# Optimization experiments

Measured on AMD Instinct MI355X. Metric: run time of the kernel, lower is better.

Reference implementation:

```python
import jax, jax.numpy as jnp
import numpy as np

VOXEL_SIZE = np.array([0.1, 0.1, 0.2], np.float32)
PC_RANGE = np.array([-51.2, -51.2, -5.0, 51.2, 51.2, 3.0], np.float32)
MAX_POINTS = 32
MAX_VOXELS = 60000  # training cap (max_voxels[0])
GRID = np.round((PC_RANGE[3:] - PC_RANGE[:3]) / VOXEL_SIZE).astype(np.int64)  # [1024,1024,40]
N_POINTS = 1_200_000


def setup_inputs() -> dict:
    key = jax.random.key(0)
    k1, k2 = jax.random.split(key)
    lo = jnp.asarray(PC_RANGE[:3] - 2.0)   # slight margin -> some out-of-range points get dropped
    hi = jnp.asarray(PC_RANGE[3:] + 2.0)
    xyz = jax.random.uniform(k1, (N_POINTS, 3), minval=lo, maxval=hi)
    feat = jax.random.uniform(k2, (N_POINTS, 1))  # reflectivity
    return {"points": jnp.concatenate([xyz, feat], axis=1)}


def reference(points):
    # Hard voxelization (deterministic): first-occurrence voxel ordering,
    # first max_points points kept per voxel, capped at max_voxels.
    # Outputs padded to static MAX_VOXELS; voxel_num gives the valid count.
    N, ndim = points.shape
    gx, gy, gz = int(GRID[0]), int(GRID[1]), int(GRID[2])
    sentinel = gx * gy * gz  # flat id for out-of-range points (sorts last)

    vs = jnp.asarray(VOXEL_SIZE)
    rmin = jnp.asarray(PC_RANGE[:3])
    c = jnp.floor((points[:, :3] - rmin) / vs).astype(jnp.int32)  # [N,3] (x,y,z)
    valid = jnp.all((c >= 0) & (c < jnp.asarray(GRID, jnp.int32)), axis=1)
    flat = jnp.where(valid, (c[:, 0] * gy + c[:, 1]) * gz + c[:, 2], sentinel)

    # stable sort -> within a voxel, points keep original order
    order = jnp.argsort(flat, stable=True)
    sflat = flat[order]
    svalid = valid[order]

    new_seg = jnp.concatenate([jnp.array([True]), sflat[1:] != sflat[:-1]])
    seg_id = jnp.cumsum(new_seg) - 1                      # segment index per sorted point
    pos = jnp.arange(N)
    seg_start = jax.lax.cummax(jnp.where(new_seg, pos, 0), axis=0)
    rank = pos - seg_start                                # slot of point within its voxel

    seg_rep = jax.ops.segment_min(order, seg_id, num_segments=N)          # first-occurrence point idx
    seg_count = jax.ops.segment_sum(svalid.astype(jnp.int32), seg_id, num_segments=N)
    seg_exists = seg_count > 0                            # real (in-range) voxel segments

    # order voxels by first occurrence (matches deterministic CUDA kernel)
    rep_key = jnp.where(seg_exists, seg_rep, N)
    vox_order = jnp.argsort(rep_key, stable=True)
    vid = jnp.zeros(N, jnp.int32).at[vox_order].set(jnp.arange(N, dtype=jnp.int32))

    # scatter points into [MAX_VOXELS, MAX_POINTS, ndim]
    pv = vid[seg_id]
    keep = svalid & (pv < MAX_VOXELS) & (rank < MAX_POINTS)
    pv_s = jnp.where(keep, pv, MAX_VOXELS)  # OOB -> dropped
    voxels = jnp.zeros((MAX_VOXELS, MAX_POINTS, ndim), points.dtype)
    voxels = voxels.at[pv_s, jnp.minimum(rank, MAX_POINTS - 1)].set(points[order], mode='drop')

    # per-voxel outputs
    seg_vid = jnp.where(seg_exists, vid, MAX_VOXELS)
    npv = jnp.zeros(MAX_VOXELS, jnp.int32).at[seg_vid].set(
        jnp.minimum(seg_count, MAX_POINTS), mode='drop')
    seg_flat = jax.ops.segment_min(sflat, seg_id, num_segments=N)
    zc = seg_flat % gz
    yc = (seg_flat // gz) % gy
    xc = seg_flat // (gy * gz)
    coors = jnp.zeros((MAX_VOXELS, 3), jnp.int32).at[seg_vid].set(
        jnp.stack([zc, yc, xc], axis=1).astype(jnp.int32), mode='drop')  # (z, y, x) like mmcv

    voxel_num = jnp.minimum(jnp.sum(seg_exists.astype(jnp.int32)), MAX_VOXELS)
    return voxels, coors, npv, voxel_num
```

## Files before the change

kernel.cpp:

```cpp
#include <hip/hip_runtime.h>
#include <stdint.h>


#define GX 1024
#define GY 1024
#define GZ 40
#define MAXV 60000
#define MAXP 32
#define HBITS 21
#define HSIZE (1u << HBITS)
#define HMASK (HSIZE - 1u)
#define CANDBIT (1 << 30)
#define TB 256
#define ITEMS 16
#define TILE (TB * ITEMS)
#define EMPTY64 0xFFFFFFFFFFFFFFFFull
#define VIDMARK 0x80000000u

#define OFF_COORS ((size_t)MAXV * MAXP * 4)
#define OFF_NPV   (OFF_COORS + (size_t)MAXV * 3)
#define OFF_VNUM  (OFF_NPV + (size_t)MAXV)

typedef unsigned long long u64;

__device__ __forceinline__ unsigned hashf(int flat) {
    return ((unsigned)flat * 2654435761u) >> (32 - HBITS);
}

__global__ void k_init(u64* __restrict__ h64, int* __restrict__ cnt2,
                       unsigned char* __restrict__ contested, int n,
                       float* __restrict__ oF) {
    int i = blockIdx.x * blockDim.x + threadIdx.x;
    int stride = gridDim.x * blockDim.x;
    for (int j = i; j < (int)HSIZE; j += stride) h64[j] = EMPTY64;
    for (int j = i; j < MAXV; j += stride) cnt2[j] = 0;
    int nw = (n + 3) / 4;
    unsigned* c4 = (unsigned*)contested;
    for (int j = i; j < nw; j += stride) c4[j] = 0;
    for (int j = i; j < MAXV * 3; j += stride) oF[OFF_COORS + j] = 0.f;
}

__device__ __forceinline__ int voxel_flat(float4 pt) {
    float fx = floorf((pt.x + 51.2f) / 0.1f);
    float fy = floorf((pt.y + 51.2f) / 0.1f);
    float fz = floorf((pt.z + 5.0f) / 0.2f);
    int cx = (int)fx, cy = (int)fy, cz = (int)fz;
    bool valid = (fx >= 0.f) & (cx < GX) & (fy >= 0.f) & (cy < GY) & (fz >= 0.f) & (cz < GZ);
    return valid ? (cx * GY + cy) * GZ + cz : -1;
}

__global__ __launch_bounds__(TB) void k_build(const float4* __restrict__ pts, int n,
                                              u64* __restrict__ h64,
                                              int* __restrict__ pslot,
                                              unsigned char* __restrict__ contested) {
    int p = blockIdx.x * blockDim.x + threadIdx.x;
    if (p >= n) return;
    float4 pt = pts[p];
    int flat = voxel_flat(pt);
    if (flat < 0) { pslot[p] = -1; return; }
    u64 want = ((u64)(unsigned)flat << 32) | (unsigned)p;
    unsigned slot = hashf(flat);
    int res = -1;
    for (int probe = 0; probe < 4096; probe++) {
        u64 cur = atomicCAS(&h64[slot], EMPTY64, want);
        if (cur == EMPTY64) { res = (int)slot | CANDBIT; break; }
        if ((unsigned)(cur >> 32) == (unsigned)flat) {
            if ((unsigned)cur > (unsigned)p) {
                u64 old = atomicMin(&h64[slot], want);
                unsigned oldrep = (unsigned)old;
                if (oldrep > (unsigned)p) {
                    contested[oldrep] = 1;
                    res = (int)slot | CANDBIT;
                } else {
                    res = (int)slot;
                }
            } else {
                res = (int)slot;
            }
            break;
        }
        slot = (slot + 1u) & HMASK;
    }
    pslot[p] = res;
}

__global__ __launch_bounds__(TB) void k_partials(const int* __restrict__ pslot,
                                                 const unsigned char* __restrict__ contested,
                                                 int n, u64* __restrict__ flagbits,
                                                 int* __restrict__ partials) {
    __shared__ int sh[TB];
    int t = threadIdx.x;
    int base = blockIdx.x * TILE;
    int s = 0;
    #pragma unroll
    for (int j = 0; j < ITEMS; j++) {
        int i = base + j * TB + t;
        int pred = 0;
        if (i < n) {
            int raw = pslot[i];
            pred = (raw >= 0) && (raw & CANDBIT) && !contested[i];
        }
        u64 m = __ballot(pred);
        if ((t & 63) == 0) flagbits[i >> 6] = m;
        s += pred;
    }
    sh[t] = s;
    __syncthreads();
    for (int off = TB / 2; off > 0; off >>= 1) {
        if (t < off) sh[t] += sh[t + off];
        __syncthreads();
    }
    if (t == 0) partials[blockIdx.x] = sh[0];
}

__global__ __launch_bounds__(1024) void k_scan(int* __restrict__ partials, int nb,
                                               float* __restrict__ oF) {
    __shared__ int sh[1024];
    int t = threadIdx.x;
    int v = (t < nb) ? partials[t] : 0;
    sh[t] = v;
    __syncthreads();
    for (int off = 1; off < 1024; off <<= 1) {
        int add = (t >= off) ? sh[t - off] : 0;
        __syncthreads();
        sh[t] += add;
        __syncthreads();
    }
    if (t < nb) partials[t] = sh[t] - v;
    if (t == 1023) {
        int total = sh[1023];
        if (total > MAXV) total = MAXV;
        oF[OFF_VNUM] = (float)total;
    }
}

__global__ __launch_bounds__(TB) void k_assign(const u64* __restrict__ flagbits,
                                               const int* __restrict__ partials,
                                               const int* __restrict__ pslot,
                                               u64* __restrict__ h64,
                                               int* __restrict__ cnt2,
                                               int* __restrict__ list,
                                               float* __restrict__ oF) {
    __shared__ int sh[TB];
    int t = threadIdx.x;
    int base = blockIdx.x * TILE;
    unsigned bits = (unsigned)((flagbits[(base >> 6) + (t >> 2)] >> ((t & 3) * 16)) & 0xFFFFull);
    int s = __popc(bits);
    sh[t] = s;
    __syncthreads();
    for (int off = 1; off < TB; off <<= 1) {
        int add = (t >= off) ? sh[t - off] : 0;
        __syncthreads();
        sh[t] += add;
        __syncthreads();
    }
    int vid = partials[blockIdx.x] + (sh[t] - s);
    int ibase = base + t * ITEMS;
    #pragma unroll
    for (int j = 0; j < ITEMS; j++) {
        if ((bits >> j) & 1) {
            if (vid < MAXV) {
                int i = ibase + j;
                int slot = pslot[i] & HMASK;
                u64 v = h64[slot];
                int flat = (int)(v >> 32);
                int zc = flat % GZ;
                int t2 = flat / GZ;
                int yc = t2 % GY;
                int xc = t2 / GY;
                size_t cOff = OFF_COORS + (size_t)vid * 3;
                oF[cOff + 0] = (float)zc;
                oF[cOff + 1] = (float)yc;
                oF[cOff + 2] = (float)xc;
                cnt2[vid] = 1;
                list[vid * MAXP] = i;
                h64[slot] = ((u64)(unsigned)flat << 32) | (VIDMARK | (unsigned)vid);
            }
            vid++;
        }
    }
}

__global__ void k_scatter(const int* __restrict__ pslot,
                          const unsigned char* __restrict__ contested,
                          const u64* __restrict__ h64,
                          int* __restrict__ cnt2, int* __restrict__ list, int n) {
    int p = blockIdx.x * blockDim.x + threadIdx.x;
    if (p >= n) return;
    int raw = pslot[p];
    if (raw < 0) return;
    if ((raw & CANDBIT) && !contested[p]) return;
    unsigned low = (unsigned)h64[raw & HMASK];
    if (!(low & VIDMARK)) return;
    int vid = (int)(low & 0x7FFFFFFFu);
    int pos = atomicAdd(&cnt2[vid], 1);
    if (pos < MAXP) list[vid * MAXP + pos] = p;
}

__global__ void k_emit(const float4* __restrict__ pts, const int* __restrict__ cnt2,
                       const int* __restrict__ list, float4* __restrict__ outVox,
                       float* __restrict__ oF) {
    int vid = blockIdx.x * blockDim.x + threadIdx.x;
    if (vid >= MAXV) return;
    int m = cnt2[vid];
    if (m > MAXP) m = MAXP;
    oF[OFF_NPV + vid] = (float)m;
    const int* lst = &list[vid * MAXP];
    const float4 zero = make_float4(0.f, 0.f, 0.f, 0.f);
    int prev = -1;
    for (int r = 0; r < MAXP; r++) {
        float4 row = zero;
        if (r < m) {
            int best = 0x7FFFFFFF;
            for (int j = 0; j < m; j++) {
                int v = lst[j];
                if (v > prev && v < best) best = v;
            }
            prev = best;
            row = pts[best];
        }
        outVox[vid * MAXP + r] = row;
    }
}

extern "C" void kernel_launch(void* const* d_in, const int* in_sizes, int n_in,
                              void* d_out, int out_size, void* d_ws, size_t ws_size,
                              hipStream_t stream) {
    int n = in_sizes[0] / 4;
    const float4* pts = (const float4*)d_in[0];

    int tb = 256;
    int nbp = (n + tb - 1) / tb;
    int nb = (n + TILE - 1) / TILE;
    int nwords = (nb * TILE) / 64;

    char* base = (char*)d_ws;
    size_t o = 0;
    int* partials = (int*)(base + o);  o += 4096 * 4;
    int* cnt2     = (int*)(base + o);  o += (size_t)MAXV * 4;
    o = (o + 255) & ~(size_t)255;
    u64* flagbits = (u64*)(base + o);  o += (size_t)nwords * 8;
    o = (o + 255) & ~(size_t)255;
    unsigned char* contested = (unsigned char*)(base + o);  o += ((size_t)n + 255) & ~(size_t)255;
    u64* h64      = (u64*)(base + o);  o += (size_t)HSIZE * 8;
    int* pslot    = (int*)(base + o);  o += (size_t)n * 4;
    int* list     = (int*)(base + o);  o += (size_t)MAXV * MAXP * 4;

    float* oF = (float*)d_out;

    k_init<<<2048, tb, 0, stream>>>(h64, cnt2, contested, n, oF);
    k_build<<<nbp, tb, 0, stream>>>(pts, n, h64, pslot, contested);
    k_partials<<<nb, TB, 0, stream>>>(pslot, contested, n, flagbits, partials);
    k_scan<<<1, 1024, 0, stream>>>(partials, nb, oF);
    k_assign<<<nb, TB, 0, stream>>>(flagbits, partials, pslot, h64, cnt2, list, oF);
    k_scatter<<<nbp, tb, 0, stream>>>(pslot, contested, h64, cnt2, list, n);
    k_emit<<<(MAXV + tb - 1) / tb, tb, 0, stream>>>(pts, cnt2, list, (float4*)d_out, oF);
}
```

Baseline: 166.3 us.

## Derive voxel ids from flag-bit popcounts instead of writing them back to the hash table

The build pass now stores each point's flat voxel index, so the assign pass reads coordinates directly instead of probing the hash table. Assign also stops writing the voxel id back into the hash slot and records the representative point in a separate array. The scatter pass instead recomputes a point's voxel id from the representative index using the block partial sum plus popcounts over the flag-bit words. Emit fills row 0 from the representative array. This removes random hash-table reads and writes from assign, at the cost of an extra per-point array write in build and a popcount loop over up to 64 words for each non-representative point.

```diff
diff --git a/kernel.cpp b/kernel.cpp
--- a/kernel.cpp
+++ b/kernel.cpp
@@ -15,7 +15,6 @@
 #define ITEMS 16
 #define TILE (TB * ITEMS)
 #define EMPTY64 0xFFFFFFFFFFFFFFFFull
-#define VIDMARK 0x80000000u
 
 #define OFF_COORS ((size_t)MAXV * MAXP * 4)
 #define OFF_NPV   (OFF_COORS + (size_t)MAXV * 3)
@@ -52,11 +51,13 @@
 __global__ __launch_bounds__(TB) void k_build(const float4* __restrict__ pts, int n,
                                               u64* __restrict__ h64,
                                               int* __restrict__ pslot,
+                                              int* __restrict__ pflat,
                                               unsigned char* __restrict__ contested) {
     int p = blockIdx.x * blockDim.x + threadIdx.x;
     if (p >= n) return;
     float4 pt = pts[p];
     int flat = voxel_flat(pt);
+    pflat[p] = flat;
     if (flat < 0) { pslot[p] = -1; return; }
     u64 want = ((u64)(unsigned)flat << 32) | (unsigned)p;
     unsigned slot = hashf(flat);
@@ -136,10 +137,9 @@
 
 __global__ __launch_bounds__(TB) void k_assign(const u64* __restrict__ flagbits,
                                                const int* __restrict__ partials,
-                                               const int* __restrict__ pslot,
-                                               u64* __restrict__ h64,
+                                               const int* __restrict__ pflat,
                                                int* __restrict__ cnt2,
-                                               int* __restrict__ list,
+                                               int* __restrict__ repidx,
                                                float* __restrict__ oF) {
     __shared__ int sh[TB];
     int t = threadIdx.x;
@@ -161,9 +161,7 @@
         if ((bits >> j) & 1) {
             if (vid < MAXV) {
                 int i = ibase + j;
-                int slot = pslot[i] & HMASK;
-                u64 v = h64[slot];
-                int flat = (int)(v >> 32);
+                int flat = pflat[i];
                 int zc = flat % GZ;
                 int t2 = flat / GZ;
                 int yc = t2 % GY;
@@ -173,8 +171,7 @@
                 oF[cOff + 1] = (float)yc;
                 oF[cOff + 2] = (float)xc;
                 cnt2[vid] = 1;
-                list[vid * MAXP] = i;
-                h64[slot] = ((u64)(unsigned)flat << 32) | (VIDMARK | (unsigned)vid);
+                repidx[vid] = i;
             }
             vid++;
         }
@@ -184,35 +181,45 @@
 __global__ void k_scatter(const int* __restrict__ pslot,
                           const unsigned char* __restrict__ contested,
                           const u64* __restrict__ h64,
+                          const u64* __restrict__ flagbits,
+                          const int* __restrict__ partials,
                           int* __restrict__ cnt2, int* __restrict__ list, int n) {
     int p = blockIdx.x * blockDim.x + threadIdx.x;
     if (p >= n) return;
     int raw = pslot[p];
     if (raw < 0) return;
     if ((raw & CANDBIT) && !contested[p]) return;
-    unsigned low = (unsigned)h64[raw & HMASK];
-    if (!(low & VIDMARK)) return;
-    int vid = (int)(low & 0x7FFFFFFFu);
+    unsigned r = (unsigned)h64[raw & HMASK];
+    int blk = (int)(r >> 12);
+    int vid = partials[blk];
+    int wbase = blk << 6;
+    int we = (int)(r >> 6);
+    for (int w = wbase; w < we; w++) vid += __popcll(flagbits[w]);
+    unsigned tail = r & 63u;
+    if (tail) vid += __popcll(flagbits[we] & ((1ull << tail) - 1ull));
+    if (vid >= MAXV) return;
     int pos = atomicAdd(&cnt2[vid], 1);
     if (pos < MAXP) list[vid * MAXP + pos] = p;
 }
 
 __global__ void k_emit(const float4* __restrict__ pts, const int* __restrict__ cnt2,
-                       const int* __restrict__ list, float4* __restrict__ outVox,
-                       float* __restrict__ oF) {
+                       const int* __restrict__ repidx, const int* __restrict__ list,
+                       float4* __restrict__ outVox, float* __restrict__ oF) {
     int vid = blockIdx.x * blockDim.x + threadIdx.x;
     if (vid >= MAXV) return;
     int m = cnt2[vid];
     if (m > MAXP) m = MAXP;
     oF[OFF_NPV + vid] = (float)m;
+    const float4 zero = make_float4(0.f, 0.f, 0.f, 0.f);
     const int* lst = &list[vid * MAXP];
-    const float4 zero = make_float4(0.f, 0.f, 0.f, 0.f);
     int prev = -1;
     for (int r = 0; r < MAXP; r++) {
         float4 row = zero;
-        if (r < m) {
+        if (r == 0 && m > 0) {
+            row = pts[repidx[vid]];
+        } else if (r < m) {
             int best = 0x7FFFFFFF;
-            for (int j = 0; j < m; j++) {
+            for (int j = 1; j < m; j++) {
                 int v = lst[j];
                 if (v > prev && v < best) best = v;
             }
@@ -238,21 +245,23 @@
     size_t o = 0;
     int* partials = (int*)(base + o);  o += 4096 * 4;
     int* cnt2     = (int*)(base + o);  o += (size_t)MAXV * 4;
+    int* repidx   = (int*)(base + o);  o += (size_t)MAXV * 4;
     o = (o + 255) & ~(size_t)255;
     u64* flagbits = (u64*)(base + o);  o += (size_t)nwords * 8;
     o = (o + 255) & ~(size_t)255;
     unsigned char* contested = (unsigned char*)(base + o);  o += ((size_t)n + 255) & ~(size_t)255;
     u64* h64      = (u64*)(base + o);  o += (size_t)HSIZE * 8;
     int* pslot    = (int*)(base + o);  o += (size_t)n * 4;
+    int* pflat    = (int*)(base + o);  o += (size_t)n * 4;
     int* list     = (int*)(base + o);  o += (size_t)MAXV * MAXP * 4;
 
     float* oF = (float*)d_out;
 
     k_init<<<2048, tb, 0, stream>>>(h64, cnt2, contested, n, oF);
-    k_build<<<nbp, tb, 0, stream>>>(pts, n, h64, pslot, contested);
+    k_build<<<nbp, tb, 0, stream>>>(pts, n, h64, pslot, pflat, contested);
     k_partials<<<nb, TB, 0, stream>>>(pslot, contested, n, flagbits, partials);
     k_scan<<<1, 1024, 0, stream>>>(partials, nb, oF);
-    k_assign<<<nb, TB, 0, stream>>>(flagbits, partials, pslot, h64, cnt2, list, oF);
-    k_scatter<<<nbp, tb, 0, stream>>>(pslot, contested, h64, cnt2, list, n);
-    k_emit<<<(MAXV + tb - 1) / tb, tb, 0, stream>>>(pts, cnt2, list, (float4*)d_out, oF);
-}
+    k_assign<<<nb, TB, 0, stream>>>(flagbits, partials, pflat, cnt2, repidx, oF);
+    k_scatter<<<nbp, tb, 0, stream>>>(pslot, contested, h64, flagbits, partials, cnt2, list, n);
+    k_emit<<<(MAXV + tb - 1) / tb, tb, 0, stream>>>(pts, cnt2, repidx, list, (float4*)d_out, oF);
+}
```

Result: no change. 169.0 us (+1.6%).
